# Performance work log

Measured on AMD Instinct MI355X. Metric: run time of the kernel, lower is better.

The kernel has to match this reference:

```python
import jax, jax.numpy as jnp
import numpy as np

N, E, D_IN, H, C = 40000, 640000, 128, 2, 64  # nodes, edges, in_channels, heads, out_channels


def setup_inputs() -> dict:
    key = jax.random.key(0)
    ks = jax.random.split(key, 8)
    x = jax.random.normal(ks[0], (N, D_IN), jnp.float32)
    edge_attr = jax.random.normal(ks[1], (E, D_IN), jnp.float32)
    edge_index = jax.random.randint(ks[2], (2, E), 0, N, dtype=jnp.int32)
    W_msg = jax.random.normal(ks[3], (D_IN, H * C), jnp.float32) / np.sqrt(D_IN)
    b_msg = jnp.zeros((H * C,), jnp.float32)
    W_edge = jax.random.normal(ks[4], (D_IN, H * C), jnp.float32) / np.sqrt(D_IN)
    b_edge = jnp.zeros((H * C,), jnp.float32)
    W_self = jax.random.normal(ks[5], (D_IN, C), jnp.float32) / np.sqrt(D_IN)
    b_self = jnp.zeros((C,), jnp.float32)
    att_msg = jax.random.normal(ks[6], (1, H, C), jnp.float32) / np.sqrt(C)
    return dict(x=x, edge_attr=edge_attr, W_msg=W_msg, b_msg=b_msg,
                W_edge=W_edge, b_edge=b_edge, W_self=W_self, b_self=b_self,
                att_msg=att_msg, edge_index=edge_index)


def reference(x, edge_attr, W_msg, b_msg, W_edge, b_edge, W_self, b_self, att_msg, edge_index):
    src, dst = edge_index[0], edge_index[1]
    # edge feature transform (also returned as updated edge_attr)
    le = edge_attr @ W_edge + b_edge                      # [E, H*C]
    # gather source nodes -> linear message + edge term (message_basic)
    m = x[src] @ W_msg + b_msg + le                       # [E, H*C]
    m = m.reshape(E, H, C)
    # additive attention: alpha = leaky_relu((m * att_msg).sum(-1))
    alpha = jax.nn.leaky_relu(jnp.sum(m * att_msg, axis=-1), 0.2)  # [E, H]
    # PyG scatter-softmax over destination segments
    amax = jax.ops.segment_max(alpha, dst, num_segments=N)        # [N, H]
    amax = jnp.where(jnp.isfinite(amax), amax, 0.0)
    ex = jnp.exp(alpha - amax[dst])
    denom = jax.ops.segment_sum(ex, dst, num_segments=N)
    a = ex / (denom[dst] + 1e-16)                                  # [E, H]
    # weighted scatter-add aggregation (aggr='add')
    agg = jax.ops.segment_sum(m * a[..., None], dst, num_segments=N)  # [N, H, C]
    # mean over heads + self linear (in_channels != out_channels -> Linear)
    out = agg.mean(axis=1) + (x @ W_self + b_self)                 # [N, C]
    return out, le
```

## Files before the change

kernel.cpp:

```cpp
#include <hip/hip_runtime.h>

#define N_NODES 40000
#define N_EDGES 640000

typedef __attribute__((ext_vector_type(8))) short short8;
typedef __attribute__((ext_vector_type(4))) float float4v;

__device__ inline short f2bf(float f) {
  unsigned u = __float_as_uint(f);
  unsigned r = (u + 0x7FFFu + ((u >> 16) & 1u)) >> 16;
  return (short)r;
}

__global__ void prep_w(const float* __restrict__ Wm, const float* __restrict__ We,
                       const float* __restrict__ Ws, short* __restrict__ WtM,
                       short* __restrict__ WtE, short* __restrict__ WtS) {
  int i = blockIdx.x * 256 + threadIdx.x;
  if (i < 16384) {
    int c = i >> 7, k = i & 127;
    WtM[c * 128 + k] = f2bf(Wm[k * 128 + c]);
  } else if (i < 32768) {
    int j = i - 16384;
    int c = j >> 7, k = j & 127;
    WtE[c * 128 + k] = f2bf(We[k * 128 + c]);
  } else {
    int j = i - 32768;
    int c = j >> 7, k = j & 127;
    WtS[c * 128 + k] = f2bf(Ws[k * 64 + c]);
  }
}

template <int NT>
__global__ __launch_bounds__(256) void gemm_rows(const float* __restrict__ A,
                                                 const short* __restrict__ Wt,
                                                 const float* __restrict__ bias,
                                                 float* __restrict__ out) {
  __shared__ short wt[NT * 16 * 136];
  for (int i = threadIdx.x; i < NT * 16 * 16; i += 256) {
    int c = i >> 4, j = i & 15;
    *(uint4*)&wt[c * 136 + j * 8] = ((const uint4*)Wt)[i];
  }
  __syncthreads();
  const int l = threadIdx.x & 63, w = threadIdx.x >> 6;
  const int lr = l & 15, q = l >> 4;
  const int row = blockIdx.x * 64 + w * 16 + lr;
  float4v acc[NT];
#pragma unroll
  for (int t = 0; t < NT; ++t) acc[t] = (float4v){0.f, 0.f, 0.f, 0.f};
  const float* ap = A + (size_t)row * 128 + q * 8;
#pragma unroll
  for (int s = 0; s < 4; ++s) {
    float4 a0 = *(const float4*)(ap + s * 32);
    float4 a1 = *(const float4*)(ap + s * 32 + 4);
    short8 af;
    af[0] = f2bf(a0.x); af[1] = f2bf(a0.y); af[2] = f2bf(a0.z); af[3] = f2bf(a0.w);
    af[4] = f2bf(a1.x); af[5] = f2bf(a1.y); af[6] = f2bf(a1.z); af[7] = f2bf(a1.w);
#pragma unroll
    for (int t = 0; t < NT; ++t) {
      short8 bf = *(const short8*)&wt[(t * 16 + lr) * 136 + s * 32 + q * 8];
      acc[t] = __builtin_amdgcn_mfma_f32_16x16x32_bf16(af, bf, acc[t], 0, 0, 0);
    }
  }
  const int orow = blockIdx.x * 64 + w * 16 + q * 4;
#pragma unroll
  for (int t = 0; t < NT; ++t) {
    int col = lr + 16 * t;
    float b = bias[col];
#pragma unroll
    for (int j = 0; j < 4; ++j)
      out[(size_t)(orow + j) * (NT * 16) + col] = acc[t][j] + b;
  }
}

__global__ __launch_bounds__(256) void edge_kernel(
    const float* __restrict__ ea, const short* __restrict__ WtE,
    const float* __restrict__ b_edge, const float* __restrict__ xm,
    const float* __restrict__ att, const int* __restrict__ src,
    float* __restrict__ le_out, float* __restrict__ alpha_out) {
  __shared__ short wt[128 * 136];
  __shared__ int sid[64];
  for (int i = threadIdx.x; i < 128 * 16; i += 256) {
    int c = i >> 4, j = i & 15;
    *(uint4*)&wt[c * 136 + j * 8] = ((const uint4*)WtE)[i];
  }
  if (threadIdx.x < 64) sid[threadIdx.x] = src[blockIdx.x * 64 + threadIdx.x];
  __syncthreads();
  const int l = threadIdx.x & 63, w = threadIdx.x >> 6;
  const int lr = l & 15, q = l >> 4;
  const int r0 = blockIdx.x * 64 + w * 16;
  float4v acc[8];
#pragma unroll
  for (int t = 0; t < 8; ++t) acc[t] = (float4v){0.f, 0.f, 0.f, 0.f};
  const float* ap = ea + (size_t)(r0 + lr) * 128 + q * 8;
#pragma unroll
  for (int s = 0; s < 4; ++s) {
    float4 a0 = *(const float4*)(ap + s * 32);
    float4 a1 = *(const float4*)(ap + s * 32 + 4);
    short8 af;
    af[0] = f2bf(a0.x); af[1] = f2bf(a0.y); af[2] = f2bf(a0.z); af[3] = f2bf(a0.w);
    af[4] = f2bf(a1.x); af[5] = f2bf(a1.y); af[6] = f2bf(a1.z); af[7] = f2bf(a1.w);
#pragma unroll
    for (int t = 0; t < 8; ++t) {
      short8 bf = *(const short8*)&wt[(t * 16 + lr) * 136 + s * 32 + q * 8];
      acc[t] = __builtin_amdgcn_mfma_f32_16x16x32_bf16(af, bf, acc[t], 0, 0, 0);
    }
  }
  const int rb = q * 4;
  int sidr[4];
#pragma unroll
  for (int j = 0; j < 4; ++j) sidr[j] = sid[w * 16 + rb + j];
  float p[8];
#pragma unroll
  for (int k = 0; k < 8; ++k) p[k] = 0.f;
#pragma unroll
  for (int t = 0; t < 8; ++t) {
    int col = lr + 16 * t;
    float b = b_edge[col];
    float av = att[col];
    int hp = (t >> 2) * 4;
#pragma unroll
    for (int j = 0; j < 4; ++j) {
      float lev = acc[t][j] + b;
      le_out[(size_t)(r0 + rb + j) * 128 + col] = lev;
      float mv = lev + xm[(size_t)sidr[j] * 128 + col];
      p[hp + j] += mv * av;
    }
  }
#pragma unroll
  for (int d = 1; d < 16; d <<= 1) {
#pragma unroll
    for (int k = 0; k < 8; ++k) p[k] += __shfl_xor(p[k], d);
  }
  if (lr < 8) {
    int j = lr >> 1, h = lr & 1;
    float v = p[h * 4 + j];
    alpha_out[(size_t)(r0 + rb + j) * 2 + h] = v > 0.f ? v : 0.2f * v;
  }
}


__global__ void hist_k(const int* __restrict__ dst, int* __restrict__ cnt,
                       int* __restrict__ rank) {
  int e = blockIdx.x * 256 + threadIdx.x;
  rank[e] = atomicAdd(&cnt[dst[e]], 1);
}

__global__ __launch_bounds__(1024) void scan_k(const int* __restrict__ cnt,
                                               int* __restrict__ ofs) {
  __shared__ int tsum[1024];
  const int t = threadIdx.x;
  const int b = t * 40;
  const int hi = min(b + 40, N_NODES);
  int s = 0;
  for (int i = b; i < hi; ++i) s += cnt[i];
  tsum[t] = s;
  __syncthreads();
  for (int d = 1; d < 1024; d <<= 1) {
    int v = (t >= d) ? tsum[t - d] : 0;
    __syncthreads();
    tsum[t] += v;
    __syncthreads();
  }
  int run = (t == 0) ? 0 : tsum[t - 1];
  for (int i = b; i < hi; ++i) { ofs[i] = run; run += cnt[i]; }
  if (t == 1023) ofs[N_NODES] = run;
}

__global__ void scatter_k(const int* __restrict__ dst, const int* __restrict__ ofs,
                          const int* __restrict__ rank, int* __restrict__ eid) {
  int e = blockIdx.x * 256 + threadIdx.x;
  eid[ofs[dst[e]] + rank[e]] = e;
}

__global__ __launch_bounds__(256) void node_agg(
    const float* __restrict__ le, const float* __restrict__ xm,
    const float* __restrict__ alp, const float* __restrict__ xs,
    const int* __restrict__ ofs, const int* __restrict__ eid,
    const int* __restrict__ src, float* __restrict__ out) {
  const int w = threadIdx.x >> 6, l = threadIdx.x & 63;
  const int n = blockIdx.x * 4 + w;
  const int beg = ofs[n];
  const int deg = ofs[n + 1] - beg;
  float acc = 0.f;
  if (deg > 0) {
    float m0 = -1e30f, m1 = -1e30f;
    for (int i = l; i < deg; i += 64) {
      int e = eid[beg + i];
      m0 = fmaxf(m0, alp[2 * e]);
      m1 = fmaxf(m1, alp[2 * e + 1]);
    }
#pragma unroll
    for (int d = 1; d < 64; d <<= 1) {
      m0 = fmaxf(m0, __shfl_xor(m0, d));
      m1 = fmaxf(m1, __shfl_xor(m1, d));
    }
    float s0 = 0.f, s1 = 0.f;
    for (int i = l; i < deg; i += 64) {
      int e = eid[beg + i];
      s0 += __expf(alp[2 * e] - m0);
      s1 += __expf(alp[2 * e + 1] - m1);
    }
#pragma unroll
    for (int d = 1; d < 64; d <<= 1) {
      s0 += __shfl_xor(s0, d);
      s1 += __shfl_xor(s1, d);
    }
    const float r0 = 1.f / (s0 + 1e-16f);
    const float r1 = 1.f / (s1 + 1e-16f);
    for (int base = 0; base < deg; base += 64) {
      int i = base + l;
      int eR = 0, sR = 0;
      float w0R = 0.f, w1R = 0.f;
      if (i < deg) {
        eR = eid[beg + i];
        sR = src[eR];
        w0R = __expf(alp[2 * eR] - m0) * r0;
        w1R = __expf(alp[2 * eR + 1] - m1) * r1;
      }
      const int c = min(64, deg - base);
      for (int j = 0; j < c; ++j) {
        int e = __shfl(eR, j);
        int s = __shfl(sR, j);
        float w0 = __shfl(w0R, j);
        float w1 = __shfl(w1R, j);
        float v0 = le[(size_t)e * 128 + l] + xm[(size_t)s * 128 + l];
        float v1 = le[(size_t)e * 128 + 64 + l] + xm[(size_t)s * 128 + 64 + l];
        acc += w0 * v0 + w1 * v1;
      }
    }
  }
  out[(size_t)n * 64 + l] = 0.5f * acc + xs[(size_t)n * 64 + l];
}

extern "C" void kernel_launch(void* const* d_in, const int* in_sizes, int n_in,
                              void* d_out, int out_size, void* d_ws, size_t ws_size,
                              hipStream_t stream) {
  const float* x      = (const float*)d_in[0];
  const float* ea     = (const float*)d_in[1];
  const float* W_msg  = (const float*)d_in[2];
  const float* b_msg  = (const float*)d_in[3];
  const float* W_edge = (const float*)d_in[4];
  const float* b_edge = (const float*)d_in[5];
  const float* W_self = (const float*)d_in[6];
  const float* b_self = (const float*)d_in[7];
  const float* att    = (const float*)d_in[8];
  const int*   eidx   = (const int*)d_in[9];
  const int* src = eidx;
  const int* dst = eidx + N_EDGES;
  float* out_p = (float*)d_out;
  float* le_p  = out_p + (size_t)N_NODES * 64;

  char* ws = (char*)d_ws;
  short* WtM  = (short*)(ws);
  short* WtE  = (short*)(ws + 32768);
  short* WtS  = (short*)(ws + 65536);
  float* xm   = (float*)(ws + 81920);
  float* xs   = (float*)(ws + 20561920);
  float* alp  = (float*)(ws + 30801920);
  int*   cnt  = (int*)(ws + 35921920);
  int*   ofs  = (int*)(ws + 36081920);
  int*   rank = (int*)(ws + 36241936);
  int*   eid  = (int*)(ws + 38801936);

  hipMemsetAsync(cnt, 0, 160000, stream);

  prep_w<<<160, 256, 0, stream>>>(W_msg, W_edge, W_self, WtM, WtE, WtS);
  gemm_rows<8><<<625, 256, 0, stream>>>(x, WtM, b_msg, xm);
  gemm_rows<4><<<625, 256, 0, stream>>>(x, WtS, b_self, xs);
  hist_k<<<2500, 256, 0, stream>>>(dst, cnt, rank);
  scan_k<<<1, 1024, 0, stream>>>(cnt, ofs);
  scatter_k<<<2500, 256, 0, stream>>>(dst, ofs, rank, eid);
  edge_kernel<<<10000, 256, 0, stream>>>(ea, WtE, b_edge, xm, att, src, le_p, alp);
  node_agg<<<10000, 256, 0, stream>>>(le_p, xm, alp, xs, ofs, eid, src, out_p);
}
```

Before: 814.0 us.

## Write bf16 messages and exp-weights in CSR order from edge kernel

The edge kernel now computes each edge's message, packs the two heads into one bf16 pair word, and writes it together with exp(alpha) directly into destination-sorted CSR slots via a precomputed position array. Node aggregation then streams these contiguous records and normalises by the summed weights, replacing the random gathers of le, xm, eid and src and the separate max and sum passes. In exchange it drops the max subtraction in the softmax, which risks overflow for large logits, and rounds messages to bf16 before aggregation. It also adds an extra write buffer of packed messages.

```diff
diff --git a/kernel.cpp b/kernel.cpp
--- a/kernel.cpp
+++ b/kernel.cpp
@@ -11,6 +11,8 @@
   unsigned r = (u + 0x7FFFu + ((u >> 16) & 1u)) >> 16;
   return (short)r;
 }
+__device__ inline float bf_lo(unsigned u) { return __uint_as_float(u << 16); }
+__device__ inline float bf_hi(unsigned u) { return __uint_as_float(u & 0xFFFF0000u); }
 
 __global__ void prep_w(const float* __restrict__ Wm, const float* __restrict__ We,
                        const float* __restrict__ Ws, short* __restrict__ WtM,
@@ -72,72 +74,6 @@
   }
 }
 
-__global__ __launch_bounds__(256) void edge_kernel(
-    const float* __restrict__ ea, const short* __restrict__ WtE,
-    const float* __restrict__ b_edge, const float* __restrict__ xm,
-    const float* __restrict__ att, const int* __restrict__ src,
-    float* __restrict__ le_out, float* __restrict__ alpha_out) {
-  __shared__ short wt[128 * 136];
-  __shared__ int sid[64];
-  for (int i = threadIdx.x; i < 128 * 16; i += 256) {
-    int c = i >> 4, j = i & 15;
-    *(uint4*)&wt[c * 136 + j * 8] = ((const uint4*)WtE)[i];
-  }
-  if (threadIdx.x < 64) sid[threadIdx.x] = src[blockIdx.x * 64 + threadIdx.x];
-  __syncthreads();
-  const int l = threadIdx.x & 63, w = threadIdx.x >> 6;
-  const int lr = l & 15, q = l >> 4;
-  const int r0 = blockIdx.x * 64 + w * 16;
-  float4v acc[8];
-#pragma unroll
-  for (int t = 0; t < 8; ++t) acc[t] = (float4v){0.f, 0.f, 0.f, 0.f};
-  const float* ap = ea + (size_t)(r0 + lr) * 128 + q * 8;
-#pragma unroll
-  for (int s = 0; s < 4; ++s) {
-    float4 a0 = *(const float4*)(ap + s * 32);
-    float4 a1 = *(const float4*)(ap + s * 32 + 4);
-    short8 af;
-    af[0] = f2bf(a0.x); af[1] = f2bf(a0.y); af[2] = f2bf(a0.z); af[3] = f2bf(a0.w);
-    af[4] = f2bf(a1.x); af[5] = f2bf(a1.y); af[6] = f2bf(a1.z); af[7] = f2bf(a1.w);
-#pragma unroll
-    for (int t = 0; t < 8; ++t) {
-      short8 bf = *(const short8*)&wt[(t * 16 + lr) * 136 + s * 32 + q * 8];
-      acc[t] = __builtin_amdgcn_mfma_f32_16x16x32_bf16(af, bf, acc[t], 0, 0, 0);
-    }
-  }
-  const int rb = q * 4;
-  int sidr[4];
-#pragma unroll
-  for (int j = 0; j < 4; ++j) sidr[j] = sid[w * 16 + rb + j];
-  float p[8];
-#pragma unroll
-  for (int k = 0; k < 8; ++k) p[k] = 0.f;
-#pragma unroll
-  for (int t = 0; t < 8; ++t) {
-    int col = lr + 16 * t;
-    float b = b_edge[col];
-    float av = att[col];
-    int hp = (t >> 2) * 4;
-#pragma unroll
-    for (int j = 0; j < 4; ++j) {
-      float lev = acc[t][j] + b;
-      le_out[(size_t)(r0 + rb + j) * 128 + col] = lev;
-      float mv = lev + xm[(size_t)sidr[j] * 128 + col];
-      p[hp + j] += mv * av;
-    }
-  }
-#pragma unroll
-  for (int d = 1; d < 16; d <<= 1) {
-#pragma unroll
-    for (int k = 0; k < 8; ++k) p[k] += __shfl_xor(p[k], d);
-  }
-  if (lr < 8) {
-    int j = lr >> 1, h = lr & 1;
-    float v = p[h * 4 + j];
-    alpha_out[(size_t)(r0 + rb + j) * 2 + h] = v > 0.f ? v : 0.2f * v;
-  }
-}
-
 
 __global__ void hist_k(const int* __restrict__ dst, int* __restrict__ cnt,
                        int* __restrict__ rank) {
@@ -166,70 +102,140 @@
   if (t == 1023) ofs[N_NODES] = run;
 }
 
-__global__ void scatter_k(const int* __restrict__ dst, const int* __restrict__ ofs,
-                          const int* __restrict__ rank, int* __restrict__ eid) {
+__global__ void pos_k(const int* __restrict__ dst, const int* __restrict__ ofs,
+                      const int* __restrict__ rank, int* __restrict__ pos) {
   int e = blockIdx.x * 256 + threadIdx.x;
-  eid[ofs[dst[e]] + rank[e]] = e;
+  pos[e] = ofs[dst[e]] + rank[e];
+}
+
+__global__ __launch_bounds__(256) void edge_kernel(
+    const float* __restrict__ ea, const short* __restrict__ WtE,
+    const float* __restrict__ b_edge, const float* __restrict__ xm,
+    const float* __restrict__ att, const int* __restrict__ src,
+    const int* __restrict__ pos, float* __restrict__ le_out,
+    float* __restrict__ wcsr, unsigned* __restrict__ mcsr) {
+  __shared__ short wt[128 * 136];
+  __shared__ int sid[64];
+  __shared__ int pid[64];
+  unsigned* mst = (unsigned*)wt;
+  for (int i = threadIdx.x; i < 128 * 16; i += 256) {
+    int c = i >> 4, j = i & 15;
+    *(uint4*)&wt[c * 136 + j * 8] = ((const uint4*)WtE)[i];
+  }
+  if (threadIdx.x < 64) {
+    sid[threadIdx.x] = src[blockIdx.x * 64 + threadIdx.x];
+    pid[threadIdx.x] = pos[blockIdx.x * 64 + threadIdx.x];
+  }
+  __syncthreads();
+  const int l = threadIdx.x & 63, w = threadIdx.x >> 6;
+  const int lr = l & 15, q = l >> 4;
+  const int r0 = blockIdx.x * 64 + w * 16;
+  float4v acc[8];
+#pragma unroll
+  for (int t = 0; t < 8; ++t) acc[t] = (float4v){0.f, 0.f, 0.f, 0.f};
+  const float* ap = ea + (size_t)(r0 + lr) * 128 + q * 8;
+#pragma unroll
+  for (int s = 0; s < 4; ++s) {
+    float4 a0 = *(const float4*)(ap + s * 32);
+    float4 a1 = *(const float4*)(ap + s * 32 + 4);
+    short8 af;
+    af[0] = f2bf(a0.x); af[1] = f2bf(a0.y); af[2] = f2bf(a0.z); af[3] = f2bf(a0.w);
+    af[4] = f2bf(a1.x); af[5] = f2bf(a1.y); af[6] = f2bf(a1.z); af[7] = f2bf(a1.w);
+#pragma unroll
+    for (int t = 0; t < 8; ++t) {
+      short8 bf = *(const short8*)&wt[(t * 16 + lr) * 136 + s * 32 + q * 8];
+      acc[t] = __builtin_amdgcn_mfma_f32_16x16x32_bf16(af, bf, acc[t], 0, 0, 0);
+    }
+  }
+  __syncthreads();
+  const int rb = q * 4;
+  int sidr[4];
+#pragma unroll
+  for (int j = 0; j < 4; ++j) sidr[j] = sid[w * 16 + rb + j];
+  float p[8];
+#pragma unroll
+  for (int k = 0; k < 8; ++k) p[k] = 0.f;
+  float mv0[4][4];
+#pragma unroll
+  for (int t = 0; t < 8; ++t) {
+    int col = lr + 16 * t;
+    float b = b_edge[col];
+    float av = att[col];
+    int hp = (t >> 2) * 4;
+#pragma unroll
+    for (int j = 0; j < 4; ++j) {
+      float lev = acc[t][j] + b;
+      le_out[(size_t)(r0 + rb + j) * 128 + col] = lev;
+      float mv = lev + xm[(size_t)sidr[j] * 128 + col];
+      p[hp + j] += mv * av;
+      if (t < 4) {
+        mv0[t][j] = mv;
+      } else {
+        unsigned u = (unsigned)(unsigned short)f2bf(mv0[t - 4][j]) |
+                     ((unsigned)(unsigned short)f2bf(mv) << 16);
+        mst[(w * 16 + rb + j) * 72 + lr + 16 * (t - 4)] = u;
+      }
+    }
+  }
+#pragma unroll
+  for (int d = 1; d < 16; d <<= 1) {
+#pragma unroll
+    for (int k = 0; k < 8; ++k) p[k] += __shfl_xor(p[k], d);
+  }
+  if (lr < 8) {
+    int j = lr >> 1, h = lr & 1;
+    float v = p[h * 4 + j];
+    float lk = v > 0.f ? v : 0.2f * v;
+    wcsr[(size_t)pid[w * 16 + rb + j] * 2 + h] = __expf(lk);
+  }
+  __syncthreads();
+  {
+    const int row = threadIdx.x >> 2, part = threadIdx.x & 3;
+    const unsigned* sp = &mst[row * 72 + part * 16];
+    uint4* dp = (uint4*)(mcsr + (size_t)pid[row] * 64 + part * 16);
+#pragma unroll
+    for (int k = 0; k < 4; ++k) dp[k] = ((const uint4*)sp)[k];
+  }
 }
 
 __global__ __launch_bounds__(256) void node_agg(
-    const float* __restrict__ le, const float* __restrict__ xm,
-    const float* __restrict__ alp, const float* __restrict__ xs,
-    const int* __restrict__ ofs, const int* __restrict__ eid,
-    const int* __restrict__ src, float* __restrict__ out) {
+    const unsigned* __restrict__ mcsr, const float* __restrict__ wcsr,
+    const float* __restrict__ xs, const int* __restrict__ ofs,
+    float* __restrict__ out) {
   const int w = threadIdx.x >> 6, l = threadIdx.x & 63;
   const int n = blockIdx.x * 4 + w;
   const int beg = ofs[n];
   const int deg = ofs[n + 1] - beg;
-  float acc = 0.f;
-  if (deg > 0) {
-    float m0 = -1e30f, m1 = -1e30f;
-    for (int i = l; i < deg; i += 64) {
-      int e = eid[beg + i];
-      m0 = fmaxf(m0, alp[2 * e]);
-      m1 = fmaxf(m1, alp[2 * e + 1]);
-    }
-#pragma unroll
-    for (int d = 1; d < 64; d <<= 1) {
-      m0 = fmaxf(m0, __shfl_xor(m0, d));
-      m1 = fmaxf(m1, __shfl_xor(m1, d));
-    }
-    float s0 = 0.f, s1 = 0.f;
-    for (int i = l; i < deg; i += 64) {
-      int e = eid[beg + i];
-      s0 += __expf(alp[2 * e] - m0);
-      s1 += __expf(alp[2 * e + 1] - m1);
-    }
-#pragma unroll
-    for (int d = 1; d < 64; d <<= 1) {
-      s0 += __shfl_xor(s0, d);
-      s1 += __shfl_xor(s1, d);
-    }
-    const float r0 = 1.f / (s0 + 1e-16f);
-    const float r1 = 1.f / (s1 + 1e-16f);
-    for (int base = 0; base < deg; base += 64) {
-      int i = base + l;
-      int eR = 0, sR = 0;
-      float w0R = 0.f, w1R = 0.f;
-      if (i < deg) {
-        eR = eid[beg + i];
-        sR = src[eR];
-        w0R = __expf(alp[2 * eR] - m0) * r0;
-        w1R = __expf(alp[2 * eR + 1] - m1) * r1;
-      }
-      const int c = min(64, deg - base);
-      for (int j = 0; j < c; ++j) {
-        int e = __shfl(eR, j);
-        int s = __shfl(sR, j);
-        float w0 = __shfl(w0R, j);
-        float w1 = __shfl(w1R, j);
-        float v0 = le[(size_t)e * 128 + l] + xm[(size_t)s * 128 + l];
-        float v1 = le[(size_t)e * 128 + 64 + l] + xm[(size_t)s * 128 + 64 + l];
-        acc += w0 * v0 + w1 * v1;
-      }
-    }
-  }
-  out[(size_t)n * 64 + l] = 0.5f * acc + xs[(size_t)n * 64 + l];
+  float acc0 = 0.f, acc1 = 0.f, den0 = 0.f, den1 = 0.f;
+  const unsigned* mp = mcsr + (size_t)beg * 64 + l;
+  const float* wp = wcsr + (size_t)beg * 2;
+  int i = 0;
+  for (; i + 4 <= deg; i += 4) {
+    unsigned u0 = mp[0], u1 = mp[64], u2 = mp[128], u3 = mp[192];
+    float wa0 = wp[0], wb0 = wp[1];
+    float wa1 = wp[2], wb1 = wp[3];
+    float wa2 = wp[4], wb2 = wp[5];
+    float wa3 = wp[6], wb3 = wp[7];
+    acc0 += wa0 * bf_lo(u0) + wa1 * bf_lo(u1) + wa2 * bf_lo(u2) + wa3 * bf_lo(u3);
+    acc1 += wb0 * bf_hi(u0) + wb1 * bf_hi(u1) + wb2 * bf_hi(u2) + wb3 * bf_hi(u3);
+    den0 += wa0 + wa1 + wa2 + wa3;
+    den1 += wb0 + wb1 + wb2 + wb3;
+    mp += 256;
+    wp += 8;
+  }
+  for (; i < deg; ++i) {
+    unsigned u = mp[0];
+    float wa = wp[0], wb = wp[1];
+    acc0 += wa * bf_lo(u);
+    acc1 += wb * bf_hi(u);
+    den0 += wa;
+    den1 += wb;
+    mp += 64;
+    wp += 2;
+  }
+  float r0 = 1.f / (den0 + 1e-16f);
+  float r1 = 1.f / (den1 + 1e-16f);
+  out[(size_t)n * 64 + l] = 0.5f * (acc0 * r0 + acc1 * r1) + xs[(size_t)n * 64 + l];
 }
 
 extern "C" void kernel_launch(void* const* d_in, const int* in_sizes, int n_in,
@@ -251,16 +257,17 @@
   float* le_p  = out_p + (size_t)N_NODES * 64;
 
   char* ws = (char*)d_ws;
-  short* WtM  = (short*)(ws);
-  short* WtE  = (short*)(ws + 32768);
-  short* WtS  = (short*)(ws + 65536);
-  float* xm   = (float*)(ws + 81920);
-  float* xs   = (float*)(ws + 20561920);
-  float* alp  = (float*)(ws + 30801920);
-  int*   cnt  = (int*)(ws + 35921920);
-  int*   ofs  = (int*)(ws + 36081920);
-  int*   rank = (int*)(ws + 36241936);
-  int*   eid  = (int*)(ws + 38801936);
+  short* WtM   = (short*)(ws);
+  short* WtE   = (short*)(ws + 32768);
+  short* WtS   = (short*)(ws + 65536);
+  float* xm    = (float*)(ws + 81920);
+  float* xs    = (float*)(ws + 20561920);
+  float* wcsr  = (float*)(ws + 30801920);
+  int*   cnt   = (int*)(ws + 35921920);
+  int*   ofs   = (int*)(ws + 36081920);
+  int*   rank  = (int*)(ws + 36241936);
+  int*   pos   = (int*)(ws + 38801936);
+  unsigned* mcsr = (unsigned*)(ws + 41361936);
 
   hipMemsetAsync(cnt, 0, 160000, stream);
 
@@ -269,7 +276,8 @@
   gemm_rows<4><<<625, 256, 0, stream>>>(x, WtS, b_self, xs);
   hist_k<<<2500, 256, 0, stream>>>(dst, cnt, rank);
   scan_k<<<1, 1024, 0, stream>>>(cnt, ofs);
-  scatter_k<<<2500, 256, 0, stream>>>(dst, ofs, rank, eid);
-  edge_kernel<<<10000, 256, 0, stream>>>(ea, WtE, b_edge, xm, att, src, le_p, alp);
-  node_agg<<<10000, 256, 0, stream>>>(le_p, xm, alp, xs, ofs, eid, src, out_p);
-}
+  pos_k<<<2500, 256, 0, stream>>>(dst, ofs, rank, pos);
+  edge_kernel<<<10000, 256, 0, stream>>>(ea, WtE, b_edge, xm, att, src, pos,
+                                         le_p, wcsr, mcsr);
+  node_agg<<<10000, 256, 0, stream>>>(mcsr, wcsr, xs, ofs, out_p);
+}
```

Result: no change. 817.4 us (+0.4%).
